# Kernel optimization log

Measured on AMD Instinct MI355X. Metric: run time of the kernel, lower is better.

## Reference

```python
import jax, jax.numpy as jnp
import numpy as np

T, B, IN, H1, HB = 512, 256, 64, 128, 32  # seq, batch, input, LSTM width, bottleneck


def _lstm(x, w_ih, w_hh, b_ih, b_hh):
    """Single-layer unidirectional LSTM, time-major x: [T,B,in] -> [T,B,H].
    PyTorch gate order: i, f, g, o. Zero initial state."""
    H = w_hh.shape[1]
    # hoist input projection out of the scan: [T,B,4H]
    xg = jnp.einsum('tbi,gi->tbg', x, w_ih) + b_ih + b_hh

    def step(carry, xt):
        h, c = carry
        g = xt + h @ w_hh.T
        i, f, gg, o = jnp.split(g, 4, axis=-1)
        c = jax.nn.sigmoid(f) * c + jax.nn.sigmoid(i) * jnp.tanh(gg)
        h = jax.nn.sigmoid(o) * jnp.tanh(c)
        return (h, c), h

    h0 = jnp.zeros((x.shape[1], H), x.dtype)
    (_, _), hs = jax.lax.scan(step, (h0, h0), xg)
    return hs


def setup_inputs() -> dict:
    key = jax.random.key(0)
    ks = jax.random.split(key, 17)
    s = 0.05

    def p(k, shape):
        return jax.random.normal(k, shape, dtype=jnp.float32) * s

    return {
        'X': jax.random.normal(ks[0], (T, B, IN), dtype=jnp.float32),
        # en1: IN -> H1
        'w1_ih': p(ks[1], (4 * H1, IN)), 'w1_hh': p(ks[2], (4 * H1, H1)),
        'b1_ih': p(ks[3], (4 * H1,)), 'b1_hh': p(ks[4], (4 * H1,)),
        # en2: H1 -> HB
        'w2_ih': p(ks[5], (4 * HB, H1)), 'w2_hh': p(ks[6], (4 * HB, HB)),
        'b2_ih': p(ks[7], (4 * HB,)), 'b2_hh': p(ks[8], (4 * HB,)),
        # de1: HB -> H1
        'w3_ih': p(ks[9], (4 * H1, HB)), 'w3_hh': p(ks[10], (4 * H1, H1)),
        'b3_ih': p(ks[11], (4 * H1,)), 'b3_hh': p(ks[12], (4 * H1,)),
        # de2: H1 -> IN
        'w4_ih': p(ks[13], (4 * IN, H1)), 'w4_hh': p(ks[14], (4 * IN, IN)),
        'b4_ih': p(ks[15], (4 * IN,)), 'b4_hh': p(ks[16], (4 * IN,)),
    }


def reference(X, w1_ih, w1_hh, b1_ih, b1_hh, w2_ih, w2_hh, b2_ih, b2_hh,
              w3_ih, w3_hh, b3_ih, b3_hh, w4_ih, w4_hh, b4_ih, b4_hh):
    h = _lstm(X, w1_ih, w1_hh, b1_ih, b1_hh)      # [T,B,128]
    h = _lstm(h, w2_ih, w2_hh, b2_ih, b2_hh)      # [T,B,32]
    h = jnp.tanh(h)                               # bottleneck tanh
    h = _lstm(h, w3_ih, w3_hh, b3_ih, b3_hh)      # [T,B,128]
    out = _lstm(h, w4_ih, w4_hh, b4_ih, b4_hh)    # [T,B,64]
    return out
```

## Files before the change

### kernel.cpp

```cpp
#include <hip/hip_runtime.h>

#define T_STEPS 512
#define BATCH   256

typedef _Float16 f16;
typedef unsigned long long u64;
typedef __attribute__((ext_vector_type(8))) _Float16 f16x8;
typedef __attribute__((ext_vector_type(4))) _Float16 f16x4;
typedef __attribute__((ext_vector_type(4))) float    f32x4;

#define L2E 1.44269504088896340736f

__device__ __forceinline__ float rcp_f(float x)  { return __builtin_amdgcn_rcpf(x); }
__device__ __forceinline__ float exp2_f(float x) { return __builtin_amdgcn_exp2f(x); }

__device__ __forceinline__ float tanh_n(float x) {
    return fmaf(-2.0f, rcp_f(1.0f + exp2_f(2.0f * L2E * x)), 1.0f);
}
__device__ __forceinline__ u64 tanh4_f16(u64 v) {
    f16x4 h = __builtin_bit_cast(f16x4, v);
    f16x4 r;
#pragma unroll
    for (int i = 0; i < 4; ++i) r[i] = (f16)tanh_n((float)h[i]);
    return __builtin_bit_cast(u64, r);
}

__device__ __forceinline__ void barrier_lgkm() {
    asm volatile("s_waitcnt lgkmcnt(0)\n\ts_barrier" ::: "memory");
}
__device__ __forceinline__ void barrier_drain() {
    asm volatile("s_waitcnt vmcnt(0) lgkmcnt(0)\n\ts_barrier" ::: "memory");
}

__device__ __forceinline__ int  flag_load(const int* p) {
    return __hip_atomic_load(p, __ATOMIC_RELAXED, __HIP_MEMORY_SCOPE_AGENT);
}
__device__ __forceinline__ void flag_store(int* p, int v) {
    __hip_atomic_store(p, v, __ATOMIC_RELAXED, __HIP_MEMORY_SCOPE_AGENT);
}
__device__ __forceinline__ u64  panel_load(const u64* p) {
    return __hip_atomic_load(p, __ATOMIC_RELAXED, __HIP_MEMORY_SCOPE_AGENT);
}
__device__ __forceinline__ void panel_store(u64* p, u64 v) {
    __hip_atomic_store(p, v, __ATOMIC_RELAXED, __HIP_MEMORY_SCOPE_AGENT);
}

template <int IN_DIM, int H, bool IN_F32, bool OUT_PANEL, bool OUT_TANH>
__device__ __forceinline__ void lstm_layer_dev(
    char* sm,
    const void* __restrict__ xv,
    const int* in_flag,
    int* out_flag,
    const float* __restrict__ w_ih, const float* __restrict__ w_hh,
    const float* __restrict__ b_ih, const float* __restrict__ b_hh,
    void* __restrict__ outv,
    int group, int ltid)
{
    constexpr int KTX = IN_DIM / 32, KTH = H / 32, KT = KTX + KTH;
    constexpr int XP = IN_DIM + 8, HP = H + 8, NT = 4 * H;

    f16 (*xs)[16][XP] = (f16(*)[16][XP])sm;
    f16 (*hs)[16][HP] = (f16(*)[16][HP])(sm + 2 * 16 * XP * 2);

    const int wave = ltid >> 6, lane = ltid & 63;
    const int col = lane & 15, q = lane >> 4;
    const int bblk = group * 16;
    const int u = wave * 16 + col;

    f16x8 bw[4][KT];
#pragma unroll
    for (int g = 0; g < 4; ++g) {
        const float sc = (g == 2) ? 2.0f * L2E : L2E;
        const int row = g * H + u;
#pragma unroll
        for (int kt = 0; kt < KTX; ++kt) {
            const float* p = w_ih + (size_t)row * IN_DIM + kt * 32 + q * 8;
            f16x8 v;
#pragma unroll
            for (int j = 0; j < 8; ++j) v[j] = (f16)(p[j] * sc);
            bw[g][kt] = v;
        }
#pragma unroll
        for (int kt = 0; kt < KTH; ++kt) {
            const float* p = w_hh + (size_t)row * H + kt * 32 + q * 8;
            f16x8 v;
#pragma unroll
            for (int j = 0; j < 8; ++j) v[j] = (f16)(p[j] * sc);
            bw[g][KTX + kt] = v;
        }
    }
    float bias[4];
#pragma unroll
    for (int g = 0; g < 4; ++g)
        bias[g] = (b_ih[g * H + u] + b_hh[g * H + u]) * ((g == 2) ? 2.0f * L2E : L2E);
    float cst[4] = {0.f, 0.f, 0.f, 0.f};

    constexpr int ELD = IN_F32 ? 4 : 8;
    constexpr int EPR = IN_DIM / ELD;
    constexpr int NCH = 16 * EPR;
    constexpr int CPT = (NCH + NT - 1) / NT;
    constexpr long XADVB = (long)BATCH * IN_DIM * (IN_F32 ? 4 : 2);
    bool sv[CPT]; const char* sgp[CPT]; f16* slp[CPT];
    constexpr int LDSD = 16 * XP;
#pragma unroll
    for (int k = 0; k < CPT; ++k) {
        const int cc = ltid + k * NT;
        sv[k] = (cc < NCH);
        const int r_ = (cc < NCH ? cc : 0) / EPR;
        const int o_ = (cc < NCH ? cc : 0) % EPR;
        sgp[k] = (const char*)xv + ((size_t)(bblk + r_) * IN_DIM + o_ * ELD) * (IN_F32 ? 4 : 2);
        slp[k] = &xs[0][r_][o_ * ELD];
    }

    constexpr int OEPR = H / 4;
    u64* opg = nullptr;
    f16* olds = nullptr;
    float* outp_f32 = nullptr;
    if constexpr (OUT_PANEL) {
        const int orow = ltid / OEPR, ooff = ltid % OEPR;
        opg  = (u64*)((f16*)outv + (size_t)(bblk + orow) * H) + ooff;
        olds = &hs[0][orow][ooff * 4];
    } else {
        outp_f32 = (float*)outv + ((size_t)bblk + 4 * q) * H + u;
    }
    constexpr int HLDSD = 16 * HP;

    for (int i = ltid; i < 16 * HP; i += NT) hs[0][i / HP][i % HP] = (f16)0.f;
    int seen = 0;
    if constexpr (!IN_F32) {
        do { seen = flag_load(in_flag); } while (seen < 1);
    }
#pragma unroll
    for (int k = 0; k < CPT; ++k) {
        if (sv[k]) {
            if constexpr (IN_F32) {
                const f32x4 v = *reinterpret_cast<const f32x4*>(sgp[k]);
                f16x4 h4;
                h4[0] = (f16)v[0]; h4[1] = (f16)v[1]; h4[2] = (f16)v[2]; h4[3] = (f16)v[3];
                *reinterpret_cast<f16x4*>(slp[k]) = h4;
            } else {
                u64 a = panel_load((const u64*)sgp[k]);
                u64 b = panel_load((const u64*)sgp[k] + 1);
                u64 pk[2] = {a, b};
                *reinterpret_cast<f16x8*>(slp[k]) = *reinterpret_cast<const f16x8*>(pk);
            }
            sgp[k] += XADVB;
        }
    }
    barrier_drain();

    float hold[4] = {0.f, 0.f, 0.f, 0.f};

    auto step = [&](int t, int pbv, bool dodrain, bool dopub) {
        if constexpr (OUT_PANEL) {
            if (dopub && t >= 4 && ltid == 0) flag_store(out_flag, t - 1);
        }

        f32x4 xr32[CPT]; u64 xr16[CPT][2];
        const bool pf = (t + 1 < T_STEPS);
        if (pf) {
            if constexpr (!IN_F32) {
                if (seen < t + 2) {
                    do { seen = flag_load(in_flag); } while (seen < t + 2);
                }
            }
#pragma unroll
            for (int k = 0; k < CPT; ++k) {
                if (sv[k]) {
                    if constexpr (IN_F32) {
                        xr32[k] = *reinterpret_cast<const f32x4*>(sgp[k]);
                    } else {
                        xr16[k][0] = panel_load((const u64*)sgp[k]);
                        xr16[k][1] = panel_load((const u64*)sgp[k] + 1);
                    }
                    sgp[k] += XADVB;
                }
            }
        }

        if (t >= 1) {
            if constexpr (OUT_PANEL) {
                u64 v = *reinterpret_cast<const u64*>(olds + pbv * HLDSD);
                if constexpr (OUT_TANH) v = tanh4_f16(v);
                panel_store(opg, v);
                opg += (size_t)BATCH * H / 4;
            } else {
#pragma unroll
                for (int r = 0; r < 4; ++r) outp_f32[r * H] = hold[r];
                outp_f32 += (size_t)BATCH * H;
            }
        }

        f16x8 a[KT];
#pragma unroll
        for (int kt = 0; kt < KTX; ++kt)
            a[kt] = *reinterpret_cast<const f16x8*>(&xs[pbv][col][kt * 32 + q * 8]);
#pragma unroll
        for (int kt = 0; kt < KTH; ++kt)
            a[KTX + kt] = *reinterpret_cast<const f16x8*>(&hs[pbv][col][kt * 32 + q * 8]);

        f32x4 acc[4];
#pragma unroll
        for (int g = 0; g < 4; ++g)
            acc[g] = (f32x4){bias[g], bias[g], bias[g], bias[g]};
#pragma unroll
        for (int kt = 0; kt < KT; ++kt)
#pragma unroll
            for (int g = 0; g < 4; ++g)
                acc[g] = __builtin_amdgcn_mfma_f32_16x16x32_f16(a[kt], bw[g][kt], acc[g], 0, 0, 0);

#pragma unroll
        for (int r = 0; r < 4; ++r) {
            const float yi = acc[0][r];
            const float yf = acc[1][r];
            const float yg = acc[2][r];
            const float yo = acc[3][r];
            const float si = rcp_f(1.0f + exp2_f(-yi));
            const float sf = rcp_f(1.0f + exp2_f(-yf));
            const float dg = rcp_f(1.0f + exp2_f(yg));
            const float tgp = fmaf(dg, -4.0f * L2E, 2.0f * L2E);
            cst[r] = fmaf(sf, cst[r], si * tgp);
            const float dc = rcp_f(1.0f + exp2_f(cst[r]));
            const float th = fmaf(-2.0f, dc, 1.0f);
            const float so = rcp_f(1.0f + exp2_f(-yo));
            const float h = so * th;
            hs[pbv ^ 1][4 * q + r][u] = (f16)h;
            if constexpr (!OUT_PANEL) hold[r] = h;
        }

        if (pf) {
#pragma unroll
            for (int k = 0; k < CPT; ++k) {
                if (sv[k]) {
                    f16* dst = slp[k] + (pbv ^ 1) * LDSD;
                    if constexpr (IN_F32) {
                        f16x4 h4;
                        h4[0] = (f16)xr32[k][0]; h4[1] = (f16)xr32[k][1];
                        h4[2] = (f16)xr32[k][2]; h4[3] = (f16)xr32[k][3];
                        *reinterpret_cast<f16x4*>(dst) = h4;
                    } else {
                        *reinterpret_cast<f16x8*>(dst) =
                            *reinterpret_cast<const f16x8*>(xr16[k]);
                    }
                }
            }
        }

        if constexpr (!IN_F32) {
            if (dopub && seen < t + 9) seen = flag_load(in_flag);
        }

        if (dodrain) barrier_drain(); else barrier_lgkm();
    };

    for (int tb = 0; tb < T_STEPS; tb += 4) {
        step(tb + 0, 0, false, true);
        step(tb + 1, 1, false, false);
        step(tb + 2, 0, false, false);
        step(tb + 3, 1, true,  false);
    }

    if constexpr (OUT_PANEL) {
        u64 v = *reinterpret_cast<const u64*>(olds);
        if constexpr (OUT_TANH) v = tanh4_f16(v);
        panel_store(opg, v);
    } else {
#pragma unroll
        for (int r = 0; r < 4; ++r) outp_f32[r * H] = hold[r];
    }
    barrier_drain();
    if constexpr (OUT_PANEL) {
        if (ltid == 0) flag_store(out_flag, T_STEPS + 4);
    }
}

__global__ __launch_bounds__(512, 1)
void lstm_fused(const float* __restrict__ X,
                const float* __restrict__ w1_ih, const float* __restrict__ w1_hh,
                const float* __restrict__ b1_ih, const float* __restrict__ b1_hh,
                const float* __restrict__ w2_ih, const float* __restrict__ w2_hh,
                const float* __restrict__ b2_ih, const float* __restrict__ b2_hh,
                const float* __restrict__ w3_ih, const float* __restrict__ w3_hh,
                const float* __restrict__ b3_ih, const float* __restrict__ b3_hh,
                const float* __restrict__ w4_ih, const float* __restrict__ w4_hh,
                const float* __restrict__ b4_ih, const float* __restrict__ b4_hh,
                f16* __restrict__ h1, f16* __restrict__ h2, f16* __restrict__ h3,
                int* __restrict__ flags, float* __restrict__ out)
{
    __shared__ __attribute__((aligned(16))) char smem[45056];
    const int b = blockIdx.x, tid = threadIdx.x;

    if (b < 16) {
        lstm_layer_dev<64, 128, true, true, false>(
            smem, X, nullptr, flags + 0 * 16 + b,
            w1_ih, w1_hh, b1_ih, b1_hh, h1, b, tid);
    } else if (b < 20) {
        const int gl = tid >> 7;
        const int g  = (b - 16) * 4 + gl;
        lstm_layer_dev<128, 32, false, true, true>(
            smem + gl * 11264, h1, flags + 0 * 16 + g, flags + 1 * 16 + g,
            w2_ih, w2_hh, b2_ih, b2_hh, h2, g, tid & 127);
    } else if (b < 36) {
        const int g = b - 20;
        lstm_layer_dev<32, 128, false, true, false>(
            smem, h2, flags + 1 * 16 + g, flags + 2 * 16 + g,
            w3_ih, w3_hh, b3_ih, b3_hh, h3, g, tid);
    } else {
        const int gl = tid >> 8;
        const int g  = (b - 36) * 2 + gl;
        lstm_layer_dev<128, 64, false, false, false>(
            smem + gl * 13312, h3, flags + 2 * 16 + g, nullptr,
            w4_ih, w4_hh, b4_ih, b4_hh, out, g, tid & 255);
    }
}

extern "C" void kernel_launch(void* const* d_in, const int* in_sizes, int n_in,
                              void* d_out, int out_size, void* d_ws, size_t ws_size,
                              hipStream_t stream) {
    const float* X     = (const float*)d_in[0];
    const float* w1_ih = (const float*)d_in[1];
    const float* w1_hh = (const float*)d_in[2];
    const float* b1_ih = (const float*)d_in[3];
    const float* b1_hh = (const float*)d_in[4];
    const float* w2_ih = (const float*)d_in[5];
    const float* w2_hh = (const float*)d_in[6];
    const float* b2_ih = (const float*)d_in[7];
    const float* b2_hh = (const float*)d_in[8];
    const float* w3_ih = (const float*)d_in[9];
    const float* w3_hh = (const float*)d_in[10];
    const float* b3_ih = (const float*)d_in[11];
    const float* b3_hh = (const float*)d_in[12];
    const float* w4_ih = (const float*)d_in[13];
    const float* w4_hh = (const float*)d_in[14];
    const float* b4_ih = (const float*)d_in[15];
    const float* b4_hh = (const float*)d_in[16];

    float* out = (float*)d_out;

    int* flags = (int*)d_ws;
    f16* h1 = (f16*)((char*)d_ws + 256);
    f16* h2 = h1 + (size_t)T_STEPS * BATCH * 128;
    f16* h3 = h2 + (size_t)T_STEPS * BATCH * 32;

    lstm_fused<<<44, 512, 0, stream>>>(X,
        w1_ih, w1_hh, b1_ih, b1_hh, w2_ih, w2_hh, b2_ih, b2_hh,
        w3_ih, w3_hh, b3_ih, b3_hh, w4_ih, w4_hh, b4_ih, b4_hh,
        h1, h2, h3, flags, out);
}
```

Baseline: 649.4 us.

## Transpose MFMA so each lane owns four hidden units and stores h directly

Swaps the MFMA operands so the accumulator holds four consecutive hidden units per lane for one batch row. Each lane then writes h as one packed f16x4 to LDS and straight to the global panel or output, replacing the deferred copy from LDS one step later. The gate math is reworked to share reciprocals across products of denominators, with a clamp on the cell state to avoid overflow. The output flag now publishes t instead of t-1, because outputs are written in the same step; this relies on the stores being visible before the flag.

```diff
diff --git a/kernel.cpp b/kernel.cpp
--- a/kernel.cpp
+++ b/kernel.cpp
@@ -16,13 +16,6 @@
 
 __device__ __forceinline__ float tanh_n(float x) {
     return fmaf(-2.0f, rcp_f(1.0f + exp2_f(2.0f * L2E * x)), 1.0f);
-}
-__device__ __forceinline__ u64 tanh4_f16(u64 v) {
-    f16x4 h = __builtin_bit_cast(f16x4, v);
-    f16x4 r;
-#pragma unroll
-    for (int i = 0; i < 4; ++i) r[i] = (f16)tanh_n((float)h[i]);
-    return __builtin_bit_cast(u64, r);
 }
 
 __device__ __forceinline__ void barrier_lgkm() {
@@ -65,7 +58,8 @@
     const int wave = ltid >> 6, lane = ltid & 63;
     const int col = lane & 15, q = lane >> 4;
     const int bblk = group * 16;
-    const int u = wave * 16 + col;
+    const int u  = wave * 16 + col;
+    const int uu = wave * 16 + 4 * q;
 
     f16x8 bw[4][KT];
 #pragma unroll
@@ -89,10 +83,14 @@
             bw[g][KTX + kt] = v;
         }
     }
-    float bias[4];
-#pragma unroll
-    for (int g = 0; g < 4; ++g)
-        bias[g] = (b_ih[g * H + u] + b_hh[g * H + u]) * ((g == 2) ? 2.0f * L2E : L2E);
+    float bias[4][4];
+#pragma unroll
+    for (int g = 0; g < 4; ++g) {
+        const float sc = (g == 2) ? 2.0f * L2E : L2E;
+#pragma unroll
+        for (int r = 0; r < 4; ++r)
+            bias[g][r] = (b_ih[g * H + uu + r] + b_hh[g * H + uu + r]) * sc;
+    }
     float cst[4] = {0.f, 0.f, 0.f, 0.f};
 
     constexpr int ELD = IN_F32 ? 4 : 8;
@@ -112,18 +110,12 @@
         slp[k] = &xs[0][r_][o_ * ELD];
     }
 
-    constexpr int OEPR = H / 4;
-    u64* opg = nullptr;
-    f16* olds = nullptr;
-    float* outp_f32 = nullptr;
-    if constexpr (OUT_PANEL) {
-        const int orow = ltid / OEPR, ooff = ltid % OEPR;
-        opg  = (u64*)((f16*)outv + (size_t)(bblk + orow) * H) + ooff;
-        olds = &hs[0][orow][ooff * 4];
-    } else {
-        outp_f32 = (float*)outv + ((size_t)bblk + 4 * q) * H + u;
-    }
-    constexpr int HLDSD = 16 * HP;
+    u64*   ppg  = nullptr;
+    float* optr = nullptr;
+    if constexpr (OUT_PANEL)
+        ppg = (u64*)((f16*)outv + ((size_t)bblk + col) * H + uu);
+    else
+        optr = (float*)outv + ((size_t)bblk + col) * H + uu;
 
     for (int i = ltid; i < 16 * HP; i += NT) hs[0][i / HP][i % HP] = (f16)0.f;
     int seen = 0;
@@ -149,11 +141,9 @@
     }
     barrier_drain();
 
-    float hold[4] = {0.f, 0.f, 0.f, 0.f};
-
     auto step = [&](int t, int pbv, bool dodrain, bool dopub) {
         if constexpr (OUT_PANEL) {
-            if (dopub && t >= 4 && ltid == 0) flag_store(out_flag, t - 1);
+            if (dopub && t >= 4 && ltid == 0) flag_store(out_flag, t);
         }
 
         f32x4 xr32[CPT]; u64 xr16[CPT][2];
@@ -178,19 +168,6 @@
             }
         }
 
-        if (t >= 1) {
-            if constexpr (OUT_PANEL) {
-                u64 v = *reinterpret_cast<const u64*>(olds + pbv * HLDSD);
-                if constexpr (OUT_TANH) v = tanh4_f16(v);
-                panel_store(opg, v);
-                opg += (size_t)BATCH * H / 4;
-            } else {
-#pragma unroll
-                for (int r = 0; r < 4; ++r) outp_f32[r * H] = hold[r];
-                outp_f32 += (size_t)BATCH * H;
-            }
-        }
-
         f16x8 a[KT];
 #pragma unroll
         for (int kt = 0; kt < KTX; ++kt)
@@ -202,30 +179,47 @@
         f32x4 acc[4];
 #pragma unroll
         for (int g = 0; g < 4; ++g)
-            acc[g] = (f32x4){bias[g], bias[g], bias[g], bias[g]};
+            acc[g] = (f32x4){bias[g][0], bias[g][1], bias[g][2], bias[g][3]};
 #pragma unroll
         for (int kt = 0; kt < KT; ++kt)
 #pragma unroll
             for (int g = 0; g < 4; ++g)
-                acc[g] = __builtin_amdgcn_mfma_f32_16x16x32_f16(a[kt], bw[g][kt], acc[g], 0, 0, 0);
-
+                acc[g] = __builtin_amdgcn_mfma_f32_16x16x32_f16(bw[g][kt], a[kt], acc[g], 0, 0, 0);
+
+        float hf[4];
+        f16x4 hv;
 #pragma unroll
         for (int r = 0; r < 4; ++r) {
-            const float yi = acc[0][r];
-            const float yf = acc[1][r];
-            const float yg = acc[2][r];
-            const float yo = acc[3][r];
-            const float si = rcp_f(1.0f + exp2_f(-yi));
-            const float sf = rcp_f(1.0f + exp2_f(-yf));
-            const float dg = rcp_f(1.0f + exp2_f(yg));
-            const float tgp = fmaf(dg, -4.0f * L2E, 2.0f * L2E);
-            cst[r] = fmaf(sf, cst[r], si * tgp);
-            const float dc = rcp_f(1.0f + exp2_f(cst[r]));
-            const float th = fmaf(-2.0f, dc, 1.0f);
-            const float so = rcp_f(1.0f + exp2_f(-yo));
-            const float h = so * th;
-            hs[pbv ^ 1][4 * q + r][u] = (f16)h;
-            if constexpr (!OUT_PANEL) hold[r] = h;
+            const float zi = exp2_f(-acc[0][r]);
+            const float zf = exp2_f(-acc[1][r]);
+            const float zg = exp2_f(acc[2][r]);
+            const float zo = exp2_f(-acc[3][r]);
+            const float d1 = rcp_f((1.0f + zi) * (1.0f + zg));
+            const float d2 = rcp_f(1.0f + zf);
+            float cn = fmaf(cst[r], d2, (2.0f * L2E) * ((zg - 1.0f) * d1));
+            cn = fminf(fmaxf(cn, -80.0f), 80.0f);
+            cst[r] = cn;
+            const float zc = exp2_f(cn);
+            const float d3 = rcp_f((zc + 1.0f) * (1.0f + zo));
+            const float h = (zc - 1.0f) * d3;
+            hf[r] = h;
+            hv[r] = (f16)h;
+        }
+
+        *reinterpret_cast<f16x4*>(&hs[pbv ^ 1][col][uu]) = hv;
+
+        if constexpr (OUT_PANEL) {
+            f16x4 pv = hv;
+            if constexpr (OUT_TANH) {
+#pragma unroll
+                for (int r = 0; r < 4; ++r) pv[r] = (f16)tanh_n(hf[r]);
+            }
+            panel_store(ppg, __builtin_bit_cast(u64, pv));
+            ppg += (size_t)BATCH * H / 4;
+        } else {
+            f32x4 ov = (f32x4){hf[0], hf[1], hf[2], hf[3]};
+            *reinterpret_cast<f32x4*>(optr) = ov;
+            optr += (size_t)BATCH * H;
         }
 
         if (pf) {
@@ -260,14 +254,6 @@
         step(tb + 3, 1, true,  false);
     }
 
-    if constexpr (OUT_PANEL) {
-        u64 v = *reinterpret_cast<const u64*>(olds);
-        if constexpr (OUT_TANH) v = tanh4_f16(v);
-        panel_store(opg, v);
-    } else {
-#pragma unroll
-        for (int r = 0; r < 4; ++r) outp_f32[r * H] = hold[r];
-    }
     barrier_drain();
     if constexpr (OUT_PANEL) {
         if (ltid == 0) flag_store(out_flag, T_STEPS + 4);
```

Result: slower. 665.5 us (+2.5%).
